# Kernel tuning notes

Measured on AMD Instinct MI355X. Metric: run time of the kernel, lower is better.

The kernel has to match this reference:

```python
import jax, jax.numpy as jnp
import numpy as np
import math

D_MODEL = 768
NUM_HEADS = 12
D_K = D_MODEL // NUM_HEADS

def setup_inputs() -> dict:
    key = jax.random.key(0)
    k_x, k_q, k_k, k_v, k_o = jax.random.split(key, 5)
    x = jax.random.normal(k_x, (2, 2048, D_MODEL), dtype=jnp.float32)
    std = math.sqrt(2.0 / (D_MODEL + D_MODEL))
    # trunc_normal approx: clip normal to [-3std, 3std]
    def tn(k):
        return jnp.clip(jax.random.normal(k, (D_MODEL, D_MODEL), dtype=jnp.float32) * std, -3 * std, 3 * std)
    return {
        "x": x,
        "weight_query": tn(k_q),
        "weight_key": tn(k_k),
        "weight_value": tn(k_v),
        "weight_output": tn(k_o),
    }

def reference(x, weight_query, weight_key, weight_value, weight_output):
    # x: (b, s, d_model); weights: (d_out, d_model)
    b, s, _ = x.shape
    def proj_heads(w):
        y = jnp.einsum('od,bsd->bso', w, x)  # (b, s, h*dk)
        return y.reshape(b, s, NUM_HEADS, D_K).transpose(0, 2, 1, 3)  # (b, h, s, dk)
    Q = proj_heads(weight_query)
    K = proj_heads(weight_key)
    V = proj_heads(weight_value)
    scores = jnp.einsum('bhqd,bhkd->bhqk', Q, K) / jnp.sqrt(jnp.asarray(D_K, x.dtype))
    causal = jnp.tril(jnp.ones((s, s), dtype=bool))  # (sq, sk)
    scores = jnp.where(causal, scores, -jnp.inf)
    attn = jax.nn.softmax(scores, axis=-1)
    out_heads = jnp.einsum('bhqk,bhkd->bhqd', attn, V)  # (b, h, s, dv)
    attn_out = out_heads.transpose(0, 2, 1, 3).reshape(b, s, NUM_HEADS * D_K)
    return jnp.einsum('di,bsi->bsd', weight_output, attn_out)
```

## Files before the change

### kernel.cpp

```cpp
#include <hip/hip_runtime.h>
#include <stdint.h>

typedef float f32x4 __attribute__((ext_vector_type(4)));
typedef __bf16 bf16x8 __attribute__((ext_vector_type(8)));
typedef uint32_t u32a  __attribute__((may_alias));
typedef uint2    u2a   __attribute__((may_alias));
typedef uint4    u4a   __attribute__((may_alias));

#define VS 2064

__device__ __forceinline__ ushort f2b(float f) {
  uint32_t u = __builtin_bit_cast(uint32_t, f);
  u += 0x7FFFu + ((u >> 16) & 1u);
  return (ushort)(u >> 16);
}
__device__ __forceinline__ uint32_t b16(uint32_t u) {
  u += 0x7FFFu + ((u >> 16) & 1u);
  return u >> 16;
}

__device__ __forceinline__ bf16x8 ld_frag(const ushort* p) {
  u4a u = *(const u4a*)p;
  return __builtin_bit_cast(bf16x8, u);
}

__device__ __forceinline__ u4a cvt8(const float* p) {
  u4a a = *(const u4a*)p, b = *(const u4a*)(p + 4), o;
  o.x = b16(a.x) | (b16(a.y) << 16);
  o.y = b16(a.z) | (b16(a.w) << 16);
  o.z = b16(b.x) | (b16(b.y) << 16);
  o.w = b16(b.z) | (b16(b.w) << 16);
  return o;
}

__device__ __forceinline__ void load_lds16(const void* g, void* l) {
  __builtin_amdgcn_global_load_lds(
      (const __attribute__((address_space(1))) uint32_t*)g,
      (__attribute__((address_space(3))) uint32_t*)l, 16, 0, 0);
}

__device__ __forceinline__ uint32_t comb2(uint32_t a, uint32_t b, float w0, float w1) {
  float lo = __builtin_bit_cast(float, a << 16) * w0 +
             __builtin_bit_cast(float, b << 16) * w1;
  float hi = __builtin_bit_cast(float, a & 0xFFFF0000u) * w0 +
             __builtin_bit_cast(float, b & 0xFFFF0000u) * w1;
  return (uint32_t)f2b(lo) | ((uint32_t)f2b(hi) << 16);
}

__global__ __launch_bounds__(256) void convert_kernel(
    const float* __restrict__ x,  const float* __restrict__ wq,
    const float* __restrict__ wk, const float* __restrict__ wv,
    const float* __restrict__ wo,
    ushort* __restrict__ xb,  ushort* __restrict__ wqb,
    ushort* __restrict__ wkb, ushort* __restrict__ wvb,
    ushort* __restrict__ wob)
{
  const size_t NX = 3145728, NW = 589824;
  size_t idx = ((size_t)blockIdx.x * 256 + threadIdx.x) * 8;
  const float* src; ushort* dst; size_t off;
  if      (idx < NX)          { src = x;  dst = xb;  off = idx; }
  else if (idx < NX + NW)     { src = wq; dst = wqb; off = idx - NX; }
  else if (idx < NX + 2 * NW) { src = wk; dst = wkb; off = idx - NX - NW; }
  else if (idx < NX + 3 * NW) { src = wv; dst = wvb; off = idx - NX - 2 * NW; }
  else                        { src = wo; dst = wob; off = idx - NX - 3 * NW; }
  *(u4a*)(dst + off) = cvt8(src + off);
}

__global__ __launch_bounds__(256) void gemm_qkv(
    const ushort* __restrict__ A,
    const ushort* __restrict__ B0, const ushort* __restrict__ B1,
    const ushort* __restrict__ B2,
    ushort* __restrict__ Qo, ushort* __restrict__ Ko, ushort* __restrict__ Vt,
    int M, int N, int K)
{
  const ushort* B = blockIdx.z == 0 ? B0 : (blockIdx.z == 1 ? B1 : B2);
  const int m0 = blockIdx.x * 128, n0 = blockIdx.y * 64;
  __shared__ ushort As[128 * 32];
  __shared__ ushort Bs[64 * 32];
  const int tid = threadIdx.x, wave = tid >> 6, lane = tid & 63;
  const int quad = lane >> 4, l16 = lane & 15;
  const int mw = (wave & 1) * 64, nw = (wave >> 1) * 32;
  f32x4 acc[4][2] = {};

  for (int k0 = 0; k0 < K; k0 += 32) {
#pragma unroll
    for (int i = 0; i < 2; ++i) {
      int c = i * 256 + tid;
      load_lds16(A + (size_t)(m0 + (c >> 2)) * K + k0 + (c & 3) * 8,
                 As + (size_t)(i * 256 + wave * 64) * 8);
    }
    load_lds16(B + (size_t)(n0 + (tid >> 2)) * K + k0 + (tid & 3) * 8,
               Bs + (size_t)(wave * 64) * 8);
    __syncthreads();
    bf16x8 af[4], bfr[2];
#pragma unroll
    for (int i = 0; i < 4; ++i) af[i]  = ld_frag(As + (mw + i * 16 + l16) * 32 + quad * 8);
#pragma unroll
    for (int j = 0; j < 2; ++j) bfr[j] = ld_frag(Bs + (nw + j * 16 + l16) * 32 + quad * 8);
#pragma unroll
    for (int i = 0; i < 4; ++i)
#pragma unroll
      for (int j = 0; j < 2; ++j)
        acc[i][j] = __builtin_amdgcn_mfma_f32_16x16x32_bf16(af[i], bfr[j], acc[i][j], 0, 0, 0);
    __syncthreads();
  }
  if (blockIdx.z < 2) {
    ushort* C = blockIdx.z == 0 ? Qo : Ko;
    const float sc = blockIdx.z == 0 ? 0.125f : 1.0f;
#pragma unroll
    for (int i = 0; i < 4; ++i)
#pragma unroll
      for (int j = 0; j < 2; ++j)
#pragma unroll
        for (int r = 0; r < 4; ++r) {
          int row = m0 + mw + i * 16 + quad * 4 + r;
          int col = n0 + nw + j * 16 + l16;
          C[(size_t)row * N + col] = f2b(acc[i][j][r] * sc);
        }
  } else {
#pragma unroll
    for (int i = 0; i < 4; ++i)
#pragma unroll
      for (int j = 0; j < 2; ++j) {
        int col = n0 + nw + j * 16 + l16;
        int h = col >> 6, dv = col & 63;
        int t = m0 + mw + i * 16 + quad * 4;
        int b = t >> 11, s = t & 2047;
        u2a pw;
        pw.x = (uint32_t)f2b(acc[i][j][0]) | ((uint32_t)f2b(acc[i][j][1]) << 16);
        pw.y = (uint32_t)f2b(acc[i][j][2]) | ((uint32_t)f2b(acc[i][j][3]) << 16);
        *(u2a*)(Vt + (((size_t)b * 12 + h) * 64 + dv) * VS + s) = pw;
      }
  }
}

__global__ __launch_bounds__(256) void gemm_out(
    const ushort* __restrict__ A, const ushort* __restrict__ B,
    float* __restrict__ C, int M, int N, int K)
{
  const int m0 = blockIdx.x * 64, n0 = blockIdx.y * 64;
  __shared__ ushort As[64 * 32];
  __shared__ ushort Bs[64 * 32];
  const int tid = threadIdx.x, wave = tid >> 6, lane = tid & 63;
  const int quad = lane >> 4, l16 = lane & 15;
  const int mw = (wave & 1) * 32, nw = (wave >> 1) * 32;
  f32x4 acc[2][2] = {};

  for (int k0 = 0; k0 < K; k0 += 32) {
    load_lds16(A + (size_t)(m0 + (tid >> 2)) * K + k0 + (tid & 3) * 8,
               As + (size_t)(wave * 64) * 8);
    load_lds16(B + (size_t)(n0 + (tid >> 2)) * K + k0 + (tid & 3) * 8,
               Bs + (size_t)(wave * 64) * 8);
    __syncthreads();
    bf16x8 af[2], bfr[2];
#pragma unroll
    for (int i = 0; i < 2; ++i) af[i]  = ld_frag(As + (mw + i * 16 + l16) * 32 + quad * 8);
#pragma unroll
    for (int j = 0; j < 2; ++j) bfr[j] = ld_frag(Bs + (nw + j * 16 + l16) * 32 + quad * 8);
#pragma unroll
    for (int i = 0; i < 2; ++i)
#pragma unroll
      for (int j = 0; j < 2; ++j)
        acc[i][j] = __builtin_amdgcn_mfma_f32_16x16x32_bf16(af[i], bfr[j], acc[i][j], 0, 0, 0);
    __syncthreads();
  }
#pragma unroll
  for (int i = 0; i < 2; ++i)
#pragma unroll
    for (int j = 0; j < 2; ++j)
#pragma unroll
      for (int r = 0; r < 4; ++r) {
        int row = m0 + mw + i * 16 + quad * 4 + r;
        int col = n0 + nw + j * 16 + l16;
        C[(size_t)row * N + col] = acc[i][j][r];
      }
}

__global__ __launch_bounds__(256) void attn_kernel(
    const ushort* __restrict__ Qb, const ushort* __restrict__ Kb,
    const ushort* __restrict__ Vt, ushort* __restrict__ Opart,
    float2* __restrict__ MLp)
{
  const int S = 2048, DM = 768;
  const int pair = blockIdx.x >> 1, j = blockIdx.x & 1;
  const int h = blockIdx.y, bb = blockIdx.z;
  const ushort* Qp  = Qb + (size_t)bb * S * DM + h * 64;
  const ushort* Kp  = Kb + (size_t)bb * S * DM + h * 64;
  const ushort* Vth = Vt + ((size_t)bb * 12 + h) * 64 * VS;

  __shared__ ushort Ks[128 * 72];
  __shared__ ushort Vs[64 * 136];
  __shared__ ushort Ps[4][16 * 136];

  const int tid = threadIdx.x, wave = tid >> 6, lane = tid & 63;
  const int quad = lane >> 4, l16 = lane & 15;
  const float LOG2E = 1.44269504f;
  const float NEG_BIG = -1.0e30f;

  for (int sp = 0; sp < 2; ++sp) {
    const int qt = sp == 0 ? pair : 31 - pair;
    const int q0 = qt * 64;
    const int qg = q0 + wave * 16 + l16;

    bf16x8 bq0 = ld_frag(Qp + (size_t)qg * DM + quad * 8);
    bf16x8 bq1 = ld_frag(Qp + (size_t)qg * DM + 32 + quad * 8);

    f32x4 acc_o[4] = {};
    float m_run = NEG_BIG, l_run = 0.0f;
    const int nkt = (qt >> 1) + 1;

    for (int kt = j; kt < nkt; kt += 2) {
      const int kk0 = kt * 128;
#pragma unroll
      for (int i = 0; i < 4; ++i) {
        int c = i * 256 + tid;
        int r = c >> 3, col = (c & 7) * 8;
        *(u4a*)(Ks + r * 72 + col) = *(const u4a*)(Kp + (size_t)(kk0 + r) * DM + col);
      }
#pragma unroll
      for (int i = 0; i < 4; ++i) {
        int c = i * 256 + tid;
        int dv = c >> 4, kc = (c & 15) * 8;
        *(u4a*)(Vs + dv * 136 + kc) = *(const u4a*)(Vth + (size_t)dv * VS + kk0 + kc);
      }
      __syncthreads();

      f32x4 sacc[8] = {};
#pragma unroll
      for (int tt = 0; tt < 8; ++tt) {
        bf16x8 ak0 = ld_frag(Ks + (tt * 16 + l16) * 72 + quad * 8);
        bf16x8 ak1 = ld_frag(Ks + (tt * 16 + l16) * 72 + 32 + quad * 8);
        sacc[tt] = __builtin_amdgcn_mfma_f32_16x16x32_bf16(ak0, bq0, sacc[tt], 0, 0, 0);
        sacc[tt] = __builtin_amdgcn_mfma_f32_16x16x32_bf16(ak1, bq1, sacc[tt], 0, 0, 0);
      }

      const bool domask = (kt == nkt - 1);
      float mt = NEG_BIG;
#pragma unroll
      for (int tt = 0; tt < 8; ++tt)
#pragma unroll
        for (int r = 0; r < 4; ++r) {
          float s = sacc[tt][r];
          if (domask) {
            int kkg = kk0 + tt * 16 + quad * 4 + r;
            if (kkg > qg) s = NEG_BIG;
          }
          sacc[tt][r] = s;
          mt = fmaxf(mt, s);
        }
      mt = fmaxf(mt, __shfl_xor(mt, 16, 64));
      mt = fmaxf(mt, __shfl_xor(mt, 32, 64));
      float mnew = fmaxf(m_run, mt);
      float alpha = exp2f((m_run - mnew) * LOG2E);
      float lsum = 0.0f;
#pragma unroll
      for (int tt = 0; tt < 8; ++tt) {
        float p0 = exp2f((sacc[tt][0] - mnew) * LOG2E);
        float p1 = exp2f((sacc[tt][1] - mnew) * LOG2E);
        float p2 = exp2f((sacc[tt][2] - mnew) * LOG2E);
        float p3 = exp2f((sacc[tt][3] - mnew) * LOG2E);
        lsum += (p0 + p1) + (p2 + p3);
        uint32_t u0 = __builtin_bit_cast(uint32_t, p0);
        uint32_t u1 = __builtin_bit_cast(uint32_t, p1);
        uint32_t u2 = __builtin_bit_cast(uint32_t, p2);
        uint32_t u3 = __builtin_bit_cast(uint32_t, p3);
        u2a pw;
        pw.x = (u0 >> 16) | (u1 & 0xFFFF0000u);
        pw.y = (u2 >> 16) | (u3 & 0xFFFF0000u);
        *(u2a*)(&Ps[wave][l16 * 136 + tt * 16 + quad * 4]) = pw;
      }
      asm volatile("s_waitcnt lgkmcnt(0)" ::: "memory");
      lsum += __shfl_xor(lsum, 16, 64);
      lsum += __shfl_xor(lsum, 32, 64);
      l_run = l_run * alpha + lsum;
      m_run = mnew;

      float ar0 = __shfl(alpha, quad * 4 + 0, 64);
      float ar1 = __shfl(alpha, quad * 4 + 1, 64);
      float ar2 = __shfl(alpha, quad * 4 + 2, 64);
      float ar3 = __shfl(alpha, quad * 4 + 3, 64);
#pragma unroll
      for (int ct = 0; ct < 4; ++ct) {
        acc_o[ct][0] *= ar0; acc_o[ct][1] *= ar1;
        acc_o[ct][2] *= ar2; acc_o[ct][3] *= ar3;
      }

#pragma unroll
      for (int ks = 0; ks < 4; ++ks) {
        bf16x8 ap = ld_frag(&Ps[wave][l16 * 136 + ks * 32 + quad * 8]);
#pragma unroll
        for (int ct = 0; ct < 4; ++ct) {
          bf16x8 bv = ld_frag(Vs + (size_t)(ct * 16 + l16) * 136 + ks * 32 + quad * 8);
          acc_o[ct] = __builtin_amdgcn_mfma_f32_16x16x32_bf16(ap, bv, acc_o[ct], 0, 0, 0);
        }
      }
      __syncthreads();
    }

    const int slot = (((bb * 12 + h) << 5) + qt) * 2 + j;
    ushort* Os = Opart + (size_t)slot * 4096;
    const int r0 = wave * 16 + quad * 4;
#pragma unroll
    for (int ct = 0; ct < 4; ++ct) {
      int col = ct * 16 + l16;
      Os[(r0 + 0) * 64 + col] = f2b(acc_o[ct][0]);
      Os[(r0 + 1) * 64 + col] = f2b(acc_o[ct][1]);
      Os[(r0 + 2) * 64 + col] = f2b(acc_o[ct][2]);
      Os[(r0 + 3) * 64 + col] = f2b(acc_o[ct][3]);
    }
    if (quad == 0)
      MLp[(size_t)slot * 64 + wave * 16 + l16] = make_float2(m_run, l_run);
  }
}

__global__ __launch_bounds__(256) void combine_kernel(
    const ushort* __restrict__ Opart, const float2* __restrict__ MLp,
    ushort* __restrict__ Ab)
{
  const int sid = blockIdx.x;
  const int bb = sid / 384, rem = sid % 384, h = rem >> 5, qt = rem & 31;
  const int t = threadIdx.x, row = t >> 2, cg = (t & 3) * 16;
  float2 ml0 = MLp[(size_t)(sid * 2) * 64 + row];
  float2 ml1 = MLp[(size_t)(sid * 2 + 1) * 64 + row];
  float ms = fmaxf(ml0.x, ml1.x);
  float w0 = exp2f((ml0.x - ms) * 1.44269504f);
  float w1 = exp2f((ml1.x - ms) * 1.44269504f);
  float inv = 1.0f / (ml0.y * w0 + ml1.y * w1);
  w0 *= inv; w1 *= inv;
  const ushort* p0 = Opart + (size_t)(sid * 2) * 4096 + row * 64 + cg;
  ushort* dst = Ab + ((size_t)(bb * 2048 + qt * 64 + row)) * 768 + h * 64 + cg;
#pragma unroll
  for (int g = 0; g < 2; ++g) {
    u4a a = *(const u4a*)(p0 + g * 8);
    u4a b = *(const u4a*)(p0 + 4096 + g * 8);
    u4a o;
    o.x = comb2(a.x, b.x, w0, w1);
    o.y = comb2(a.y, b.y, w0, w1);
    o.z = comb2(a.z, b.z, w0, w1);
    o.w = comb2(a.w, b.w, w0, w1);
    *(u4a*)(dst + g * 8) = o;
  }
}

extern "C" void kernel_launch(void* const* d_in, const int* in_sizes, int n_in,
                              void* d_out, int out_size, void* d_ws, size_t ws_size,
                              hipStream_t stream) {
  (void)in_sizes; (void)n_in; (void)out_size; (void)ws_size;
  const float* x  = (const float*)d_in[0];
  const float* wq = (const float*)d_in[1];
  const float* wk = (const float*)d_in[2];
  const float* wv = (const float*)d_in[3];
  const float* wo = (const float*)d_in[4];

  const size_t NT = (size_t)4096 * 768;
  const size_t NW = (size_t)768 * 768;
  const size_t NV = (size_t)24 * 64 * VS;
  ushort* xb    = (ushort*)d_ws;
  ushort* Qbuf  = xb + NT;
  ushort* Kbuf  = Qbuf + NT;
  ushort* Vt    = Kbuf + NT;
  ushort* wqb   = Vt + NV;
  ushort* wkb   = wqb + NW;
  ushort* wvb   = wkb + NW;
  ushort* wob   = wvb + NW;
  ushort* Opart = wob + NW;
  float2* MLp   = (float2*)(Opart + (size_t)1536 * 4096);
  ushort* Abuf  = xb;

  convert_kernel<<<2688, 256, 0, stream>>>(x, wq, wk, wv, wo,
                                           xb, wqb, wkb, wvb, wob);
  gemm_qkv<<<dim3(32, 12, 3), 256, 0, stream>>>(
      xb, wqb, wkb, wvb, Qbuf, Kbuf, Vt, 4096, 768, 768);
  attn_kernel<<<dim3(32, 12, 2), 256, 0, stream>>>(Qbuf, Kbuf, Vt, Opart, MLp);
  combine_kernel<<<768, 256, 0, stream>>>(Opart, MLp, Abuf);
  gemm_out<<<dim3(64, 12), 256, 0, stream>>>(
      Abuf, wob, (float*)d_out, 4096, 768, 768);
}
```

Baseline: 174.4 us.

## Share K/V tiles across both causal query strips and deepen GEMM k-tiles

The attention kernel now processes its two paired query tiles (pair and 31-pair) together in one loop over key tiles. Each K/V tile loaded into shared memory is used by both strips instead of being reloaded in a second pass. The QKV and output projection GEMMs now step K by 64 per iteration instead of 32, halving the number of barriers and load phases. The cost is more live registers (two sets of accumulators and Q fragments) and larger shared-memory tiles, which may reduce occupancy.

```diff
diff --git a/kernel.cpp b/kernel.cpp
--- a/kernel.cpp
+++ b/kernel.cpp
@@ -75,33 +75,42 @@
 {
   const ushort* B = blockIdx.z == 0 ? B0 : (blockIdx.z == 1 ? B1 : B2);
   const int m0 = blockIdx.x * 128, n0 = blockIdx.y * 64;
-  __shared__ ushort As[128 * 32];
-  __shared__ ushort Bs[64 * 32];
+  __shared__ ushort As[128 * 64];
+  __shared__ ushort Bs[64 * 64];
   const int tid = threadIdx.x, wave = tid >> 6, lane = tid & 63;
   const int quad = lane >> 4, l16 = lane & 15;
   const int mw = (wave & 1) * 64, nw = (wave >> 1) * 32;
   f32x4 acc[4][2] = {};
 
-  for (int k0 = 0; k0 < K; k0 += 32) {
+  for (int k0 = 0; k0 < K; k0 += 64) {
+#pragma unroll
+    for (int i = 0; i < 4; ++i) {
+      int c = i * 256 + tid;
+      load_lds16(A + (size_t)(m0 + (c >> 3)) * K + k0 + (c & 7) * 8,
+                 As + (size_t)(i * 256 + wave * 64) * 8);
+    }
 #pragma unroll
     for (int i = 0; i < 2; ++i) {
       int c = i * 256 + tid;
-      load_lds16(A + (size_t)(m0 + (c >> 2)) * K + k0 + (c & 3) * 8,
-                 As + (size_t)(i * 256 + wave * 64) * 8);
-    }
-    load_lds16(B + (size_t)(n0 + (tid >> 2)) * K + k0 + (tid & 3) * 8,
-               Bs + (size_t)(wave * 64) * 8);
-    __syncthreads();
-    bf16x8 af[4], bfr[2];
-#pragma unroll
-    for (int i = 0; i < 4; ++i) af[i]  = ld_frag(As + (mw + i * 16 + l16) * 32 + quad * 8);
-#pragma unroll
-    for (int j = 0; j < 2; ++j) bfr[j] = ld_frag(Bs + (nw + j * 16 + l16) * 32 + quad * 8);
-#pragma unroll
-    for (int i = 0; i < 4; ++i)
+      load_lds16(B + (size_t)(n0 + (c >> 3)) * K + k0 + (c & 7) * 8,
+                 Bs + (size_t)(i * 256 + wave * 64) * 8);
+    }
+    __syncthreads();
+#pragma unroll
+    for (int ks = 0; ks < 2; ++ks) {
+      bf16x8 af[4], bfr[2];
+#pragma unroll
+      for (int i = 0; i < 4; ++i)
+        af[i]  = ld_frag(As + (mw + i * 16 + l16) * 64 + ks * 32 + quad * 8);
 #pragma unroll
       for (int j = 0; j < 2; ++j)
-        acc[i][j] = __builtin_amdgcn_mfma_f32_16x16x32_bf16(af[i], bfr[j], acc[i][j], 0, 0, 0);
+        bfr[j] = ld_frag(Bs + (nw + j * 16 + l16) * 64 + ks * 32 + quad * 8);
+#pragma unroll
+      for (int i = 0; i < 4; ++i)
+#pragma unroll
+        for (int j = 0; j < 2; ++j)
+          acc[i][j] = __builtin_amdgcn_mfma_f32_16x16x32_bf16(af[i], bfr[j], acc[i][j], 0, 0, 0);
+    }
     __syncthreads();
   }
   if (blockIdx.z < 2) {
@@ -139,29 +148,38 @@
     float* __restrict__ C, int M, int N, int K)
 {
   const int m0 = blockIdx.x * 64, n0 = blockIdx.y * 64;
-  __shared__ ushort As[64 * 32];
-  __shared__ ushort Bs[64 * 32];
+  __shared__ ushort As[64 * 64];
+  __shared__ ushort Bs[64 * 64];
   const int tid = threadIdx.x, wave = tid >> 6, lane = tid & 63;
   const int quad = lane >> 4, l16 = lane & 15;
   const int mw = (wave & 1) * 32, nw = (wave >> 1) * 32;
   f32x4 acc[2][2] = {};
 
-  for (int k0 = 0; k0 < K; k0 += 32) {
-    load_lds16(A + (size_t)(m0 + (tid >> 2)) * K + k0 + (tid & 3) * 8,
-               As + (size_t)(wave * 64) * 8);
-    load_lds16(B + (size_t)(n0 + (tid >> 2)) * K + k0 + (tid & 3) * 8,
-               Bs + (size_t)(wave * 64) * 8);
-    __syncthreads();
-    bf16x8 af[2], bfr[2];
-#pragma unroll
-    for (int i = 0; i < 2; ++i) af[i]  = ld_frag(As + (mw + i * 16 + l16) * 32 + quad * 8);
-#pragma unroll
-    for (int j = 0; j < 2; ++j) bfr[j] = ld_frag(Bs + (nw + j * 16 + l16) * 32 + quad * 8);
-#pragma unroll
-    for (int i = 0; i < 2; ++i)
+  for (int k0 = 0; k0 < K; k0 += 64) {
+#pragma unroll
+    for (int i = 0; i < 2; ++i) {
+      int c = i * 256 + tid;
+      load_lds16(A + (size_t)(m0 + (c >> 3)) * K + k0 + (c & 7) * 8,
+                 As + (size_t)(i * 256 + wave * 64) * 8);
+      load_lds16(B + (size_t)(n0 + (c >> 3)) * K + k0 + (c & 7) * 8,
+                 Bs + (size_t)(i * 256 + wave * 64) * 8);
+    }
+    __syncthreads();
+#pragma unroll
+    for (int ks = 0; ks < 2; ++ks) {
+      bf16x8 af[2], bfr[2];
+#pragma unroll
+      for (int i = 0; i < 2; ++i)
+        af[i]  = ld_frag(As + (mw + i * 16 + l16) * 64 + ks * 32 + quad * 8);
 #pragma unroll
       for (int j = 0; j < 2; ++j)
-        acc[i][j] = __builtin_amdgcn_mfma_f32_16x16x32_bf16(af[i], bfr[j], acc[i][j], 0, 0, 0);
+        bfr[j] = ld_frag(Bs + (nw + j * 16 + l16) * 64 + ks * 32 + quad * 8);
+#pragma unroll
+      for (int i = 0; i < 2; ++i)
+#pragma unroll
+        for (int j = 0; j < 2; ++j)
+          acc[i][j] = __builtin_amdgcn_mfma_f32_16x16x32_bf16(af[i], bfr[j], acc[i][j], 0, 0, 0);
+    }
     __syncthreads();
   }
 #pragma unroll
@@ -197,34 +215,37 @@
   const float LOG2E = 1.44269504f;
   const float NEG_BIG = -1.0e30f;
 
-  for (int sp = 0; sp < 2; ++sp) {
-    const int qt = sp == 0 ? pair : 31 - pair;
-    const int q0 = qt * 64;
-    const int qg = q0 + wave * 16 + l16;
-
-    bf16x8 bq0 = ld_frag(Qp + (size_t)qg * DM + quad * 8);
-    bf16x8 bq1 = ld_frag(Qp + (size_t)qg * DM + 32 + quad * 8);
-
-    f32x4 acc_o[4] = {};
-    float m_run = NEG_BIG, l_run = 0.0f;
-    const int nkt = (qt >> 1) + 1;
-
-    for (int kt = j; kt < nkt; kt += 2) {
-      const int kk0 = kt * 128;
-#pragma unroll
-      for (int i = 0; i < 4; ++i) {
-        int c = i * 256 + tid;
-        int r = c >> 3, col = (c & 7) * 8;
-        *(u4a*)(Ks + r * 72 + col) = *(const u4a*)(Kp + (size_t)(kk0 + r) * DM + col);
-      }
-#pragma unroll
-      for (int i = 0; i < 4; ++i) {
-        int c = i * 256 + tid;
-        int dv = c >> 4, kc = (c & 15) * 8;
-        *(u4a*)(Vs + dv * 136 + kc) = *(const u4a*)(Vth + (size_t)dv * VS + kk0 + kc);
-      }
-      __syncthreads();
-
+  const int qtA = pair, qtB = 31 - pair;
+  const int qgA = qtA * 64 + wave * 16 + l16;
+  const int qgB = qtB * 64 + wave * 16 + l16;
+  const int nktA = (qtA >> 1) + 1, nktB = (qtB >> 1) + 1;
+
+  bf16x8 bqA0 = ld_frag(Qp + (size_t)qgA * DM + quad * 8);
+  bf16x8 bqA1 = ld_frag(Qp + (size_t)qgA * DM + 32 + quad * 8);
+  bf16x8 bqB0 = ld_frag(Qp + (size_t)qgB * DM + quad * 8);
+  bf16x8 bqB1 = ld_frag(Qp + (size_t)qgB * DM + 32 + quad * 8);
+
+  f32x4 accA[4] = {}, accB[4] = {};
+  float mA = NEG_BIG, lA = 0.0f, mB = NEG_BIG, lB = 0.0f;
+
+  for (int kt = j; kt < nktB; kt += 2) {
+    const int kk0 = kt * 128;
+#pragma unroll
+    for (int i = 0; i < 4; ++i) {
+      int c = i * 256 + tid;
+      int r = c >> 3, col = (c & 7) * 8;
+      *(u4a*)(Ks + r * 72 + col) = *(const u4a*)(Kp + (size_t)(kk0 + r) * DM + col);
+    }
+#pragma unroll
+    for (int i = 0; i < 4; ++i) {
+      int c = i * 256 + tid;
+      int dv = c >> 4, kc = (c & 15) * 8;
+      *(u4a*)(Vs + dv * 136 + kc) = *(const u4a*)(Vth + (size_t)dv * VS + kk0 + kc);
+    }
+    __syncthreads();
+
+    auto strip = [&](const bf16x8& bq0, const bf16x8& bq1, f32x4* acc_o,
+                     float& m_run, float& l_run, int qg, int nkt) {
       f32x4 sacc[8] = {};
 #pragma unroll
       for (int tt = 0; tt < 8; ++tt) {
@@ -233,7 +254,6 @@
         sacc[tt] = __builtin_amdgcn_mfma_f32_16x16x32_bf16(ak0, bq0, sacc[tt], 0, 0, 0);
         sacc[tt] = __builtin_amdgcn_mfma_f32_16x16x32_bf16(ak1, bq1, sacc[tt], 0, 0, 0);
       }
-
       const bool domask = (kt == nkt - 1);
       float mt = NEG_BIG;
 #pragma unroll
@@ -274,7 +294,6 @@
       lsum += __shfl_xor(lsum, 32, 64);
       l_run = l_run * alpha + lsum;
       m_run = mnew;
-
       float ar0 = __shfl(alpha, quad * 4 + 0, 64);
       float ar1 = __shfl(alpha, quad * 4 + 1, 64);
       float ar2 = __shfl(alpha, quad * 4 + 2, 64);
@@ -284,7 +303,6 @@
         acc_o[ct][0] *= ar0; acc_o[ct][1] *= ar1;
         acc_o[ct][2] *= ar2; acc_o[ct][3] *= ar3;
       }
-
 #pragma unroll
       for (int ks = 0; ks < 4; ++ks) {
         bf16x8 ap = ld_frag(&Ps[wave][l16 * 136 + ks * 32 + quad * 8]);
@@ -294,22 +312,43 @@
           acc_o[ct] = __builtin_amdgcn_mfma_f32_16x16x32_bf16(ap, bv, acc_o[ct], 0, 0, 0);
         }
       }
-      __syncthreads();
-    }
-
-    const int slot = (((bb * 12 + h) << 5) + qt) * 2 + j;
+    };
+
+    strip(bqB0, bqB1, accB, mB, lB, qgB, nktB);
+    if (kt < nktA)
+      strip(bqA0, bqA1, accA, mA, lA, qgA, nktA);
+    __syncthreads();
+  }
+
+  const int base = ((bb * 12 + h) << 5);
+  const int r0 = wave * 16 + quad * 4;
+  {
+    const int slot = (base + qtB) * 2 + j;
     ushort* Os = Opart + (size_t)slot * 4096;
-    const int r0 = wave * 16 + quad * 4;
 #pragma unroll
     for (int ct = 0; ct < 4; ++ct) {
       int col = ct * 16 + l16;
-      Os[(r0 + 0) * 64 + col] = f2b(acc_o[ct][0]);
-      Os[(r0 + 1) * 64 + col] = f2b(acc_o[ct][1]);
-      Os[(r0 + 2) * 64 + col] = f2b(acc_o[ct][2]);
-      Os[(r0 + 3) * 64 + col] = f2b(acc_o[ct][3]);
+      Os[(r0 + 0) * 64 + col] = f2b(accB[ct][0]);
+      Os[(r0 + 1) * 64 + col] = f2b(accB[ct][1]);
+      Os[(r0 + 2) * 64 + col] = f2b(accB[ct][2]);
+      Os[(r0 + 3) * 64 + col] = f2b(accB[ct][3]);
     }
     if (quad == 0)
-      MLp[(size_t)slot * 64 + wave * 16 + l16] = make_float2(m_run, l_run);
+      MLp[(size_t)slot * 64 + wave * 16 + l16] = make_float2(mB, lB);
+  }
+  {
+    const int slot = (base + qtA) * 2 + j;
+    ushort* Os = Opart + (size_t)slot * 4096;
+#pragma unroll
+    for (int ct = 0; ct < 4; ++ct) {
+      int col = ct * 16 + l16;
+      Os[(r0 + 0) * 64 + col] = f2b(accA[ct][0]);
+      Os[(r0 + 1) * 64 + col] = f2b(accA[ct][1]);
+      Os[(r0 + 2) * 64 + col] = f2b(accA[ct][2]);
+      Os[(r0 + 3) * 64 + col] = f2b(accA[ct][3]);
+    }
+    if (quad == 0)
+      MLp[(size_t)slot * 64 + wave * 16 + l16] = make_float2(mA, lA);
   }
 }
 
```

New measurement: 173.0 us. About the same (-0.8%).
